# Optimization experiments

Hardware: AMD Instinct MI355X
Metric: run time of the kernel (lower is better)

## Reference

```python
import jax, jax.numpy as jnp
import numpy as np
from jax import lax

B, DIM, H, W = 16, 256, 32, 32
C = DIM // 4          # per-branch channels = 64
HEADS, DH = 8, 64
INNER = HEADS * DH    # 512
R = 16                # SE / CBAM channel reduction
PX = PY = 8           # learned param grid size


def _coords(n_in, n_out):
    s = jnp.linspace(0.0, n_in - 1.0, n_out)
    i0 = jnp.clip(jnp.floor(s).astype(jnp.int32), 0, max(n_in - 2, 0))
    return i0, jnp.clip(i0 + 1, 0, n_in - 1), s - i0


def resize_ac(p, out_h, out_w):
    # bilinear resize with align_corners=True; p: [..., h, w]
    y0, y1, fy = _coords(p.shape[-2], out_h)
    x0, x1, fx = _coords(p.shape[-1], out_w)
    py = p[..., y0, :] * (1.0 - fy)[:, None] + p[..., y1, :] * fy[:, None]
    return py[..., x0] * (1.0 - fx) + py[..., x1] * fx


def ln_last(x, w, b, eps=1e-5):  # torch nn.LayerNorm default eps
    m = x.mean(-1, keepdims=True)
    v = ((x - m) ** 2).mean(-1, keepdims=True)
    return (x - m) * lax.rsqrt(v + eps) * w + b


def ln_cf(x, w, b, eps=1e-6):  # channels_first ConvNeXt LayerNorm
    m = x.mean(1, keepdims=True)
    v = ((x - m) ** 2).mean(1, keepdims=True)
    return w[None, :, None, None] * ((x - m) * lax.rsqrt(v + eps)) + b[None, :, None, None]


def dwconv2d(x, w, b):  # depthwise 3x3, stride 1, pad 1
    o = lax.conv_general_dilated(x, w, (1, 1), 'SAME', dimension_numbers=('NCHW', 'OIHW', 'NCHW'), feature_group_count=x.shape[1])
    return o + b[None, :, None, None]


def dwconv1d(x, w, b):  # depthwise k=3, pad 1
    o = lax.conv_general_dilated(x, w, (1,), 'SAME', dimension_numbers=('NCH', 'OIH', 'NCH'), feature_group_count=x.shape[1])
    return o + b[None, :, None]


def pw(x, w, b):  # 1x1 conv over NCHW, w: [Cout, Cin]
    return jnp.einsum('bchw,dc->bdhw', x, w) + b[None, :, None, None]


def gelu(t):
    return jax.nn.gelu(t, approximate=False)  # torch nn.GELU default = erf


def attention(x, lnw, lnb, wqkv, wout):
    # x: [B, N, C]
    xn = ln_last(x, lnw, lnb)
    q, k, v = jnp.split(xn @ wqkv, 3, axis=-1)
    sp = lambda t: t.reshape(t.shape[0], t.shape[1], HEADS, DH).transpose(0, 2, 1, 3)
    q, k, v = sp(q), sp(k), sp(v)
    a = jax.nn.softmax(jnp.einsum('bhnd,bhmd->bhnm', q, k) * DH ** -0.5, axis=-1)
    o = jnp.einsum('bhnm,bhmd->bhnd', a, v).transpose(0, 2, 1, 3).reshape(x.shape[0], x.shape[1], INNER)
    return o @ wout


def cbam(x, fc1, fc2, sa_w):
    mlp = lambda t: jax.nn.relu(t @ fc1.T) @ fc2.T
    ca = jax.nn.sigmoid(mlp(x.mean((2, 3))) + mlp(x.max((2, 3))))
    x = x * ca[:, :, None, None]
    sp = jnp.stack([x.mean(1), x.max(1)], axis=1)  # [B,2,H,W]
    sa = lax.conv_general_dilated(sp, sa_w, (1, 1), 'SAME', dimension_numbers=('NCHW', 'OIHW', 'NCHW'))
    return x * jax.nn.sigmoid(sa)


def se(x, fc1, fc2):
    y = jax.nn.sigmoid(jax.nn.relu(x.mean((2, 3)) @ fc1.T) @ fc2.T)
    return x * y[:, :, None, None]


def setup_inputs() -> dict:
    key = jax.random.key(0)
    ks = iter(jax.random.split(key, 40))
    nrm = lambda shape, s=0.05: jax.random.normal(next(ks), shape, jnp.float32) * s
    d = {}
    d['x'] = jax.random.normal(next(ks), (B, DIM, H, W), jnp.float32)
    d['n1_w'] = jnp.ones((DIM,)); d['n1_b'] = jnp.zeros((DIM,))
    d['att_ln_w'] = jnp.ones((C,)); d['att_ln_b'] = jnp.zeros((C,))
    d['att_wqkv'] = nrm((C, 3 * INNER))
    d['att_wout'] = nrm((INNER, C))
    d['params_xy'] = jnp.ones((1, C, PX, PY))
    d['cxy_dw_w'] = nrm((C, 1, 3, 3)); d['cxy_dw_b'] = jnp.zeros((C,))
    d['cxy_pw_w'] = nrm((C, C)); d['cxy_pw_b'] = jnp.zeros((C,))
    d['ca_fc1'] = nrm((C // R, C)); d['ca_fc2'] = nrm((C, C // R))
    d['sa_w'] = nrm((1, 2, 7, 7))
    d['params_zx'] = jnp.ones((1, 1, C, PX))
    d['czx_dw_w'] = nrm((C, 1, 3)); d['czx_dw_b'] = jnp.zeros((C,))
    d['czx_pw_w'] = nrm((C, C)); d['czx_pw_b'] = jnp.zeros((C,))
    d['se_fc1'] = nrm((C // R, C)); d['se_fc2'] = nrm((C, C // R))
    d['params_zy'] = jnp.ones((1, 1, C, PY))
    d['czy_dw_w'] = nrm((C, 1, 3)); d['czy_dw_b'] = jnp.zeros((C,))
    d['czy_pw_w'] = nrm((C, C)); d['czy_pw_b'] = jnp.zeros((C,))
    d['dw_pw_w'] = nrm((C, C)); d['dw_pw_b'] = jnp.zeros((C,))
    d['dw_dw_w'] = nrm((C, 1, 3, 3)); d['dw_dw_b'] = jnp.zeros((C,))
    d['n2_w'] = jnp.ones((DIM,)); d['n2_b'] = jnp.zeros((DIM,))
    d['ldw_dw_w'] = nrm((DIM, 1, 3, 3)); d['ldw_dw_b'] = jnp.zeros((DIM,))
    d['ldw_pw_w'] = nrm((DIM, DIM)); d['ldw_pw_b'] = jnp.zeros((DIM,))
    return d


def reference(x, n1_w, n1_b, att_ln_w, att_ln_b, att_wqkv, att_wout, params_xy, cxy_dw_w, cxy_dw_b, cxy_pw_w, cxy_pw_b, ca_fc1, ca_fc2, sa_w, params_zx, czx_dw_w, czx_dw_b, czx_pw_w, czx_pw_b, se_fc1, se_fc2, params_zy, czy_dw_w, czy_dw_b, czy_pw_w, czy_pw_b, dw_pw_w, dw_pw_b, dw_dw_w, dw_dw_b, n2_w, n2_b, ldw_dw_w, ldw_dw_b, ldw_pw_w, ldw_pw_b):
    xn = ln_cf(x, n1_w, n1_b)
    x1, x2, x3, x4 = jnp.split(xn, 4, axis=1)
    Bz, Cz, Hz, Wz = x1.shape
    # branch 1: token self-attention, gated by conv'd upsampled learned grid
    t = attention(x1.transpose(0, 2, 3, 1).reshape(Bz, Hz * Wz, Cz), att_ln_w, att_ln_b, att_wqkv, att_wout)
    x1 = t.reshape(Bz, Hz, Wz, Cz).transpose(0, 3, 1, 2)
    g = pw(gelu(dwconv2d(resize_ac(params_xy, Hz, Wz), cxy_dw_w, cxy_dw_b)), cxy_pw_w, cxy_pw_b)
    x1 = x1 * g
    # branch 2: CBAM + zx gate (permute trick == broadcast over width)
    x2 = cbam(x2, ca_fc1, ca_fc2, sa_w)
    g = resize_ac(params_zx, Cz, Hz)[0]  # [1, C, H]
    g = jnp.einsum('bcl,dc->bdl', gelu(dwconv1d(g, czx_dw_w, czx_dw_b)), czx_pw_w) + czx_pw_b[None, :, None]
    x2 = x2 * g[:, :, :, None]
    # branch 3: SE + zy gate (broadcast over height)
    x3 = se(x3, se_fc1, se_fc2)
    g = resize_ac(params_zy, Cz, Wz)[0]  # [1, C, W]
    g = jnp.einsum('bcl,dc->bdl', gelu(dwconv1d(g, czy_dw_w, czy_dw_b)), czy_pw_w) + czy_pw_b[None, :, None]
    x3 = x3 * g[:, :, None, :]
    # branch 4: pointwise -> GELU -> depthwise
    x4 = dwconv2d(gelu(pw(x4, dw_pw_w, dw_pw_b)), dw_dw_w, dw_dw_b)
    out = ln_cf(jnp.concatenate([x1, x2, x3, x4], axis=1), n2_w, n2_b)
    return pw(gelu(dwconv2d(out, ldw_dw_w, ldw_dw_b)), ldw_pw_w, ldw_pw_b)
```

## Files before the change

### kernel.cpp

```cpp
#include <hip/hip_runtime.h>
#include <hip/hip_bf16.h>
#include <math.h>

#define B_     16
#define DIM_   256
#define H_     32
#define W_     32
#define HW_    1024
#define C_     64
#define HEADS_ 8
#define DH_    64
#define INNER_ 512
#define TOK_   16384

typedef unsigned short ushort_t;
typedef __bf16 bf16x8 __attribute__((ext_vector_type(8)));
typedef float  f32x4  __attribute__((ext_vector_type(4)));

#define AOFF_N1W     0
#define AOFF_N1B     256
#define AOFF_ALNW    512
#define AOFF_ALNB    576
#define AOFF_WQKV    640
#define AOFF_WOUT    98944
#define AOFF_PXY     131712
#define AOFF_CXYDW   135808
#define AOFF_CXYDWB  136384
#define AOFF_CXYPW   136448
#define AOFF_CXYPWB  140544
#define AOFF_CAF1    140608
#define AOFF_CAF2    140864
#define AOFF_SAW     141120
#define AOFF_PZX     141218
#define AOFF_CZXDW   141730
#define AOFF_CZXDWB  141922
#define AOFF_CZXPW   141986
#define AOFF_CZXPWB  146082
#define AOFF_SEF1    146146
#define AOFF_SEF2    146402
#define AOFF_PZY     146658
#define AOFF_CZYDW   147170
#define AOFF_CZYDWB  147362
#define AOFF_CZYPW   147426
#define AOFF_CZYPWB  151522
#define AOFF_DWPW    151586
#define AOFF_DWPWB   155682
#define AOFF_DWDW    155746
#define AOFF_DWDWB   156322
#define AOFF_N2W     156386
#define AOFF_N2B     156642
#define AOFF_LDWDW   156898
#define AOFF_LDWDWB  159202
#define AOFF_LDWPW   159458
#define AOFF_LDWPWB  224994
#define ATOTAL       225250

__device__ __forceinline__ float us2f(ushort_t u) {
  union { unsigned int i; float f; } v; v.i = ((unsigned int)u) << 16; return v.f;
}
__device__ __forceinline__ ushort_t f2us(float f) {
  union { float f; unsigned int i; } v; v.f = f;
  unsigned int x = v.i;
  return (ushort_t)((x + 0x7fffu + ((x >> 16) & 1u)) >> 16);
}
__device__ __forceinline__ float ldx(const void* p, size_t i, bool f32) {
  return f32 ? ((const float*)p)[i] : us2f(((const ushort_t*)p)[i]);
}
__device__ __forceinline__ float gelu_f(float x) {
  return 0.5f * x * (1.0f + erff(x * 0.70710678118654752f));
}
__device__ __forceinline__ float sigmoid_f(float x) {
  return 1.0f / (1.0f + __expf(-x));
}

__global__ void k_probe(const ushort_t* __restrict__ x, int* __restrict__ dtf) {
  __shared__ int cnt;
  if (threadIdx.x == 0) cnt = 0;
  __syncthreads();
  int c = 0;
  for (int i = threadIdx.x; i < 2048; i += 256) {
    int e = (x[i] >> 7) & 0xFF;
    if (e >= 160) ++c;
  }
  atomicAdd(&cnt, c);
  __syncthreads();
  if (threadIdx.x == 0) dtf[0] = (cnt > 16) ? 1 : 0;
}

__global__ void k_diag(void* __restrict__ out, const int* __restrict__ dtf, float val) {
  bool f32 = dtf[0] != 0;
  int i = blockIdx.x * 256 + threadIdx.x;
  if (i < B_ * DIM_ * HW_) {
    if (f32) ((float*)out)[i] = val; else ((ushort_t*)out)[i] = f2us(val);
  }
}

__global__ void k_cvt_all(const void* p0,const void* p1,const void* p2,const void* p3,const void* p4,
                          const void* p5,const void* p6,const void* p7,const void* p8,const void* p9,
                          const void* p10,const void* p11,const void* p12,const void* p13,const void* p14,
                          const void* p15,const void* p16,const void* p17,const void* p18,const void* p19,
                          const void* p20,const void* p21,const void* p22,const void* p23,const void* p24,
                          const void* p25,const void* p26,const void* p27,const void* p28,const void* p29,
                          const void* p30,const void* p31,const void* p32,const void* p33,const void* p34,
                          const void* p35, const int* __restrict__ dtf, float* __restrict__ arena) {
  const void* ps[36] = {p0,p1,p2,p3,p4,p5,p6,p7,p8,p9,p10,p11,p12,p13,p14,p15,p16,p17,
                        p18,p19,p20,p21,p22,p23,p24,p25,p26,p27,p28,p29,p30,p31,p32,p33,p34,p35};
  const int offs[37] = {AOFF_N1W,AOFF_N1B,AOFF_ALNW,AOFF_ALNB,AOFF_WQKV,AOFF_WOUT,AOFF_PXY,
    AOFF_CXYDW,AOFF_CXYDWB,AOFF_CXYPW,AOFF_CXYPWB,AOFF_CAF1,AOFF_CAF2,AOFF_SAW,AOFF_PZX,
    AOFF_CZXDW,AOFF_CZXDWB,AOFF_CZXPW,AOFF_CZXPWB,AOFF_SEF1,AOFF_SEF2,AOFF_PZY,AOFF_CZYDW,
    AOFF_CZYDWB,AOFF_CZYPW,AOFF_CZYPWB,AOFF_DWPW,AOFF_DWPWB,AOFF_DWDW,AOFF_DWDWB,AOFF_N2W,
    AOFF_N2B,AOFF_LDWDW,AOFF_LDWDWB,AOFF_LDWPW,AOFF_LDWPWB,ATOTAL};
  bool f32 = dtf[0] != 0;
  int gid = blockIdx.x * 256 + threadIdx.x;
  if (gid >= ATOTAL) return;
  int t = 0;
  while (offs[t + 1] <= gid) ++t;
  int loc = gid - offs[t];
  arena[gid] = f32 ? ((const float*)ps[t])[loc] : us2f(((const ushort_t*)ps[t])[loc]);
}

__global__ void k_wprep(const float* __restrict__ arena, ushort_t* __restrict__ wqkvT,
                        ushort_t* __restrict__ woutT, ushort_t* __restrict__ wpwB) {
  int gid = blockIdx.x * 256 + threadIdx.x;
  if (gid < 98304) {
    int j = gid >> 6, c = gid & 63;
    wqkvT[gid] = f2us(arena[AOFF_WQKV + c * 1536 + j]);
  } else if (gid < 131072) {
    int g = gid - 98304;
    int c = g >> 9, j = g & 511;
    woutT[g] = f2us(arena[AOFF_WOUT + j * 64 + c]);
  } else if (gid < 196608) {
    int g = gid - 131072;
    wpwB[g] = f2us(arena[AOFF_LDWPW + g]);
  }
}

__global__ __launch_bounds__(256) void k_ln1stats(const void* __restrict__ x, const int* __restrict__ dtf,
                                                  float* __restrict__ m1, float* __restrict__ r1) {
  __shared__ float ps[4][64], ps2[4][64];
  bool xf = dtf[0] != 0;
  int t = threadIdx.x;
  int pi = t & 63, p = t >> 6;
  int pix = blockIdx.x * 64 + pi;
  int bb = pix >> 10, hw = pix & 1023;
  size_t base = (size_t)bb * (DIM_ * HW_) + hw;
  float s = 0.f, s2 = 0.f;
  for (int c = 0; c < 64; ++c) {
    float v = ldx(x, base + (size_t)(p * 64 + c) * HW_, xf);
    s += v; s2 += v * v;
  }
  ps[p][pi] = s; ps2[p][pi] = s2;
  __syncthreads();
  if (t < 64) {
    float S = ps[0][t] + ps[1][t] + ps[2][t] + ps[3][t];
    float S2 = ps2[0][t] + ps2[1][t] + ps2[2][t] + ps2[3][t];
    float mean = S * (1.0f / DIM_);
    float var = fmaxf(S2 * (1.0f / DIM_) - mean * mean, 0.f);
    int px = blockIdx.x * 64 + t;
    m1[px] = mean;
    r1[px] = rsqrtf(var + 1e-6f);
  }
}

__global__ __launch_bounds__(256) void k_ln_tok(const void* __restrict__ x, const int* __restrict__ dtf,
                                                const float* __restrict__ m1, const float* __restrict__ r1,
                                                const float* __restrict__ arena, ushort_t* __restrict__ x1ln) {
  __shared__ float ls[64 * 65];
  __shared__ float pm[4][64], pv[4][64];
  __shared__ float mt[64], rt[64];
  bool xf = dtf[0] != 0;
  int t = threadIdx.x;
  int bb = blockIdx.x >> 4, hw0 = (blockIdx.x & 15) * 64;
  #pragma unroll
  for (int i = 0; i < 16; ++i) {
    int ch = i * 4 + (t >> 6);
    int tk = t & 63;
    int tokg = bb * HW_ + hw0 + tk;
    float v = ldx(x, ((size_t)bb * DIM_ + ch) * HW_ + hw0 + tk, xf);
    ls[ch * 65 + tk] = (v - m1[tokg]) * r1[tokg] * arena[AOFF_N1W + ch] + arena[AOFF_N1B + ch];
  }
  __syncthreads();
  {
    int p = t >> 6, tk = t & 63;
    float s = 0.f, s2 = 0.f;
    #pragma unroll
    for (int c = 0; c < 16; ++c) {
      float v = ls[(p * 16 + c) * 65 + tk];
      s += v; s2 += v * v;
    }
    pm[p][tk] = s; pv[p][tk] = s2;
  }
  __syncthreads();
  if (t < 64) {
    float S = pm[0][t] + pm[1][t] + pm[2][t] + pm[3][t];
    float S2 = pv[0][t] + pv[1][t] + pv[2][t] + pv[3][t];
    float m = S * (1.0f / C_);
    float var = fmaxf(S2 * (1.0f / C_) - m * m, 0.f);
    mt[t] = m;
    rt[t] = rsqrtf(var + 1e-5f);
  }
  __syncthreads();
  unsigned int* dst = (unsigned int*)x1ln;
  #pragma unroll
  for (int i = 0; i < 8; ++i) {
    int idx = i * 256 + t;
    int tok = idx >> 5, cp = idx & 31, c = cp * 2;
    float m = mt[tok], r = rt[tok];
    float v0 = (ls[c * 65 + tok] - m) * r * arena[AOFF_ALNW + c] + arena[AOFF_ALNB + c];
    float v1 = (ls[(c + 1) * 65 + tok] - m) * r * arena[AOFF_ALNW + c + 1] + arena[AOFF_ALNB + c + 1];
    int tokg = bb * HW_ + hw0 + tok;
    dst[(tokg * 64 + c) >> 1] = (unsigned int)f2us(v0) | ((unsigned int)f2us(v1) << 16);
  }
}

__global__ __launch_bounds__(256) void k_qkv_mfma(const ushort_t* __restrict__ x1ln,
                                                  const ushort_t* __restrict__ wqkvT,
                                                  ushort_t* __restrict__ q, ushort_t* __restrict__ k_,
                                                  ushort_t* __restrict__ v_, int tok_base) {
  int jc = blockIdx.x % 6;
  int mt = blockIdx.x / 6;
  int w = threadIdx.x >> 6, lane = threadIdx.x & 63;
  int m = lane & 15, quad = lane >> 4;
  int tok0 = mt * 64;
  bf16x8 a[4][2];
  #pragma unroll
  for (int s = 0; s < 4; ++s)
    #pragma unroll
    for (int kc = 0; kc < 2; ++kc)
      a[s][kc] = *(const bf16x8*)(x1ln + (size_t)(tok_base + tok0 + s*16 + m) * 64 + kc*32 + quad*8);
  bf16x8 bfr[4][2];
  #pragma unroll
  for (int nb = 0; nb < 4; ++nb)
    #pragma unroll
    for (int kc = 0; kc < 2; ++kc)
      bfr[nb][kc] = *(const bf16x8*)(wqkvT + (size_t)(jc*256 + w*64 + nb*16 + m) * 64 + kc*32 + quad*8);
  f32x4 cacc[4][4];
  #pragma unroll
  for (int s = 0; s < 4; ++s)
    #pragma unroll
    for (int nb = 0; nb < 4; ++nb) cacc[s][nb] = (f32x4){0.f, 0.f, 0.f, 0.f};
  #pragma unroll
  for (int kc = 0; kc < 2; ++kc)
    #pragma unroll
    for (int s = 0; s < 4; ++s)
      #pragma unroll
      for (int nb = 0; nb < 4; ++nb)
        cacc[s][nb] = __builtin_amdgcn_mfma_f32_16x16x32_bf16(a[s][kc], bfr[nb][kc], cacc[s][nb], 0, 0, 0);
  #pragma unroll
  for (int nb = 0; nb < 4; ++nb) {
    int j = jc*256 + w*64 + nb*16 + m;
    int which = j >> 9, jj = j & 511;
    int h = jj >> 6, d = jj & 63;
    ushort_t* dst = (which == 0) ? q : ((which == 1) ? k_ : v_);
    float sc = (which == 0) ? 0.125f : 1.0f;
    #pragma unroll
    for (int s = 0; s < 4; ++s)
      #pragma unroll
      for (int r = 0; r < 4; ++r) {
        int tl = tok0 + s*16 + quad*4 + r;
        int bl = tl >> 10, n = tl & 1023;
        dst[(((size_t)bl * HEADS_ + h) * 1024 + n) * 64 + d] = f2us(cacc[s][nb][r] * sc);
      }
  }
}

#define KSTR 72
__global__ __launch_bounds__(256) void k_flash_mfma(const ushort_t* __restrict__ q,
                                                    const ushort_t* __restrict__ k_,
                                                    const ushort_t* __restrict__ v_,
                                                    ushort_t* __restrict__ ao) {
  __shared__ ushort_t Kl[64 * KSTR];
  __shared__ ushort_t Vt[64 * KSTR];
  __shared__ ushort_t Pl[256 * KSTR];
  int bh = blockIdx.x >> 2;
  int qt = blockIdx.x & 3;
  int w = threadIdx.x >> 6, lane = threadIdx.x & 63;
  int m = lane & 15, quad = lane >> 4;
  const size_t bh_off = (size_t)bh * 1024 * 64;

  bf16x8 aq[4][2];
  #pragma unroll
  for (int s = 0; s < 4; ++s)
    #pragma unroll
    for (int kc = 0; kc < 2; ++kc)
      aq[s][kc] = *(const bf16x8*)(q + bh_off + (size_t)(qt*256 + w*64 + s*16 + m) * 64 + kc*32 + quad*8);

  f32x4 oacc[4][4];
  float lacc[4][4];
  #pragma unroll
  for (int s = 0; s < 4; ++s)
    #pragma unroll
    for (int i = 0; i < 4; ++i) {
      oacc[s][i] = (f32x4){0.f, 0.f, 0.f, 0.f};
      lacc[s][i] = 0.f;
    }

  int kkey = threadIdx.x & 63;
  int kd0  = (threadIdx.x >> 6) * 16;
  int vkey = (threadIdx.x & 31) * 2;
  int vd0  = (threadIdx.x >> 5) * 8;

  for (int kt = 0; kt < 16; ++kt) {
    __syncthreads();
    {
      const uint4* src = (const uint4*)(k_ + bh_off + (size_t)(kt*64 + kkey)*64 + kd0);
      uint4 u0 = src[0], u1 = src[1];
      uint4* dst = (uint4*)&Kl[kkey * KSTR + kd0];
      dst[0] = u0; dst[1] = u1;
    }
    {
      const ushort4* s0 = (const ushort4*)(v_ + bh_off + (size_t)(kt*64 + vkey)*64 + vd0);
      const ushort4* s1 = (const ushort4*)(v_ + bh_off + (size_t)(kt*64 + vkey + 1)*64 + vd0);
      ushort4 x0 = s0[0], x1 = s0[1];
      ushort4 y0 = s1[0], y1 = s1[1];
      unsigned int* base = (unsigned int*)&Vt[0];
      int col = vkey >> 1;
      base[(vd0+0)*(KSTR/2) + col] = (unsigned int)x0.x | ((unsigned int)y0.x << 16);
      base[(vd0+1)*(KSTR/2) + col] = (unsigned int)x0.y | ((unsigned int)y0.y << 16);
      base[(vd0+2)*(KSTR/2) + col] = (unsigned int)x0.z | ((unsigned int)y0.z << 16);
      base[(vd0+3)*(KSTR/2) + col] = (unsigned int)x0.w | ((unsigned int)y0.w << 16);
      base[(vd0+4)*(KSTR/2) + col] = (unsigned int)x1.x | ((unsigned int)y1.x << 16);
      base[(vd0+5)*(KSTR/2) + col] = (unsigned int)x1.y | ((unsigned int)y1.y << 16);
      base[(vd0+6)*(KSTR/2) + col] = (unsigned int)x1.z | ((unsigned int)y1.z << 16);
      base[(vd0+7)*(KSTR/2) + col] = (unsigned int)x1.w | ((unsigned int)y1.w << 16);
    }
    __syncthreads();

    f32x4 sacc[4][4];
    #pragma unroll
    for (int s = 0; s < 4; ++s)
      #pragma unroll
      for (int kb = 0; kb < 4; ++kb) sacc[s][kb] = (f32x4){0.f, 0.f, 0.f, 0.f};
    #pragma unroll
    for (int kb = 0; kb < 4; ++kb) {
      bf16x8 bk0 = *(const bf16x8*)&Kl[(kb*16 + m) * KSTR + quad*8];
      bf16x8 bk1 = *(const bf16x8*)&Kl[(kb*16 + m) * KSTR + 32 + quad*8];
      #pragma unroll
      for (int s = 0; s < 4; ++s) {
        sacc[s][kb] = __builtin_amdgcn_mfma_f32_16x16x32_bf16(aq[s][0], bk0, sacc[s][kb], 0, 0, 0);
        sacc[s][kb] = __builtin_amdgcn_mfma_f32_16x16x32_bf16(aq[s][1], bk1, sacc[s][kb], 0, 0, 0);
      }
    }

    #pragma unroll
    for (int s = 0; s < 4; ++s) {
      float rs0 = 0.f, rs1 = 0.f, rs2 = 0.f, rs3 = 0.f;
      #pragma unroll
      for (int kb = 0; kb < 4; ++kb) {
        float p0 = __expf(fminf(sacc[s][kb][0], 30.f));
        float p1 = __expf(fminf(sacc[s][kb][1], 30.f));
        float p2 = __expf(fminf(sacc[s][kb][2], 30.f));
        float p3 = __expf(fminf(sacc[s][kb][3], 30.f));
        rs0 += p0; rs1 += p1; rs2 += p2; rs3 += p3;
        int rbase = (w*64 + s*16 + quad*4) * KSTR + kb*16 + m;
        Pl[rbase + 0*KSTR] = f2us(p0);
        Pl[rbase + 1*KSTR] = f2us(p1);
        Pl[rbase + 2*KSTR] = f2us(p2);
        Pl[rbase + 3*KSTR] = f2us(p3);
      }
      #pragma unroll
      for (int mask = 1; mask <= 8; mask <<= 1) {
        rs0 += __shfl_xor(rs0, mask, 64);
        rs1 += __shfl_xor(rs1, mask, 64);
        rs2 += __shfl_xor(rs2, mask, 64);
        rs3 += __shfl_xor(rs3, mask, 64);
      }
      lacc[s][0] += rs0; lacc[s][1] += rs1; lacc[s][2] += rs2; lacc[s][3] += rs3;
    }

    bf16x8 ap[4][2];
    #pragma unroll
    for (int s = 0; s < 4; ++s)
      #pragma unroll
      for (int kc = 0; kc < 2; ++kc)
        ap[s][kc] = *(const bf16x8*)&Pl[(w*64 + s*16 + m) * KSTR + kc*32 + quad*8];
    #pragma unroll
    for (int db = 0; db < 4; ++db) {
      bf16x8 bv0 = *(const bf16x8*)&Vt[(db*16 + m) * KSTR + quad*8];
      bf16x8 bv1 = *(const bf16x8*)&Vt[(db*16 + m) * KSTR + 32 + quad*8];
      #pragma unroll
      for (int s = 0; s < 4; ++s) {
        oacc[s][db] = __builtin_amdgcn_mfma_f32_16x16x32_bf16(ap[s][0], bv0, oacc[s][db], 0, 0, 0);
        oacc[s][db] = __builtin_amdgcn_mfma_f32_16x16x32_bf16(ap[s][1], bv1, oacc[s][db], 0, 0, 0);
      }
    }
  }

  int bl = bh >> 3, h = bh & 7;
  #pragma unroll
  for (int s = 0; s < 4; ++s) {
    #pragma unroll
    for (int r = 0; r < 4; ++r) {
      float inv = 1.0f / lacc[s][r];
      int qrow = qt*256 + w*64 + s*16 + quad*4 + r;
      ushort_t* op = ao + ((size_t)(bl*1024 + qrow)) * INNER_ + h*64 + m;
      #pragma unroll
      for (int db = 0; db < 4; ++db) op[db*16] = f2us(oacc[s][db][r] * inv);
    }
  }
}

__global__ __launch_bounds__(256) void k_outproj_mfma(const ushort_t* __restrict__ ao,
                                                      const ushort_t* __restrict__ woutT,
                                                      const float* __restrict__ g1,
                                                      ushort_t* __restrict__ cat, int tok_base) {
  int w = threadIdx.x >> 6, lane = threadIdx.x & 63;
  int m = lane & 15, quad = lane >> 4;
  int tok0 = blockIdx.x * 64 + w * 16;
  f32x4 cacc[4];
  #pragma unroll
  for (int nb = 0; nb < 4; ++nb) cacc[nb] = (f32x4){0.f, 0.f, 0.f, 0.f};
  for (int kc = 0; kc < 16; ++kc) {
    bf16x8 a = *(const bf16x8*)(ao + (size_t)(tok0 + m) * INNER_ + kc*32 + quad*8);
    #pragma unroll
    for (int nb = 0; nb < 4; ++nb) {
      bf16x8 b = *(const bf16x8*)(woutT + (size_t)(nb*16 + m) * INNER_ + kc*32 + quad*8);
      cacc[nb] = __builtin_amdgcn_mfma_f32_16x16x32_bf16(a, b, cacc[nb], 0, 0, 0);
    }
  }
  #pragma unroll
  for (int nb = 0; nb < 4; ++nb) {
    int c = nb*16 + m;
    #pragma unroll
    for (int r = 0; r < 4; ++r) {
      int tokg = tok_base + tok0 + quad*4 + r;
      int bb = tokg >> 10, hw = tokg & 1023;
      cat[((size_t)bb * DIM_ + c) * HW_ + hw] = f2us(cacc[nb][r] * g1[c * HW_ + hw]);
    }
  }
}

__global__ void k_resize_xy(const float* __restrict__ arena, float* __restrict__ r) {
  const float* p = arena + AOFF_PXY;
  int idx = blockIdx.x * 256 + threadIdx.x;
  int c = idx >> 10, hw = idx & 1023, oy = hw >> 5, ox = hw & 31;
  float sy = oy * (7.0f / 31.0f); int y0 = (int)floorf(sy); y0 = y0 > 6 ? 6 : y0; float fy = sy - y0;
  float sx = ox * (7.0f / 31.0f); int x0 = (int)floorf(sx); x0 = x0 > 6 ? 6 : x0; float fx = sx - x0;
  const float* pc = p + c * 64;
  float a  = pc[y0*8+x0] * (1.f-fy) + pc[(y0+1)*8+x0] * fy;
  float b2 = pc[y0*8+x0+1] * (1.f-fy) + pc[(y0+1)*8+x0+1] * fy;
  r[idx] = a * (1.f - fx) + b2 * fx;
}
__global__ void k_dwg_xy(const float* __restrict__ r, const float* __restrict__ arena,
                         float* __restrict__ t1) {
  const float* w = arena + AOFF_CXYDW;
  const float* b = arena + AOFF_CXYDWB;
  int idx = blockIdx.x * 256 + threadIdx.x;
  int c = idx >> 10, hw = idx & 1023, yy = hw >> 5, xx = hw & 31;
  const float* base = r + c * HW_;
  float acc = b[c];
  #pragma unroll
  for (int ky = 0; ky < 3; ++ky) {
    int ny = yy + ky - 1; if (ny < 0 || ny > 31) continue;
    #pragma unroll
    for (int kx = 0; kx < 3; ++kx) {
      int nx = xx + kx - 1; if (nx < 0 || nx > 31) continue;
      acc += w[c*9 + ky*3 + kx] * base[ny*32 + nx];
    }
  }
  t1[idx] = gelu_f(acc);
}
__global__ void k_pw_xy(const float* __restrict__ t1, const float* __restrict__ arena,
                        float* __restrict__ g1) {
  const float* w = arena + AOFF_CXYPW;
  const float* b = arena + AOFF_CXYPWB;
  int idx = blockIdx.x * 256 + threadIdx.x;
  int d = idx >> 10, hw = idx & 1023;
  float acc = b[d];
  for (int c = 0; c < C_; ++c) acc += w[d*C_ + c] * t1[c*HW_ + hw];
  g1[idx] = acc;
}

__global__ void k_gate1d_a(const float* __restrict__ arena, int po, int wo, int bo,
                           float* __restrict__ t) {
  const float* p   = arena + po;
  const float* dww = arena + wo;
  const float* dwb = arena + bo;
  int idx = blockIdx.x * 256 + threadIdx.x;
  if (idx >= C_ * 32) return;
  int c = idx >> 5, i = idx & 31;
  float acc = dwb[c];
  #pragma unroll
  for (int kk = 0; kk < 3; ++kk) {
    int ii = i + kk - 1;
    if (ii < 0 || ii > 31) continue;
    float s = ii * (7.0f / 31.0f); int x0 = (int)floorf(s); x0 = x0 > 6 ? 6 : x0; float f = s - x0;
    float val = p[c*8 + x0] * (1.f - f) + p[c*8 + x0 + 1] * f;
    acc += dww[c*3 + kk] * val;
  }
  t[idx] = gelu_f(acc);
}
__global__ void k_gate1d_b(const float* __restrict__ t, const float* __restrict__ arena,
                           int wo, int bo, float* __restrict__ g) {
  const float* w = arena + wo;
  const float* b = arena + bo;
  int idx = blockIdx.x * 256 + threadIdx.x;
  if (idx >= C_ * 32) return;
  int d = idx >> 5, i = idx & 31;
  float acc = b[d];
  for (int c = 0; c < C_; ++c) acc += w[d*C_ + c] * t[c*32 + i];
  g[idx] = acc;
}

__global__ __launch_bounds__(256) void k_pool(const void* __restrict__ x, const int* __restrict__ dtf,
                                              const float* __restrict__ m1, const float* __restrict__ r1,
                                              const float* __restrict__ arena,
                                              int coff, float* __restrict__ om, float* __restrict__ ox) {
  __shared__ float sm[256], sx[256];
  bool xf = dtf[0] != 0;
  int blk = blockIdx.x;
  int bb = blk >> 6, c = blk & 63;
  const size_t xbase = ((size_t)bb * DIM_ + coff + c) * HW_;
  const float* mb = m1 + bb * HW_;
  const float* rb = r1 + bb * HW_;
  float wc = arena[AOFF_N1W + coff + c], bc = arena[AOFF_N1B + coff + c];
  int tid = threadIdx.x;
  float s = 0.f, mx = -1e30f;
  for (int i = tid; i < HW_; i += 256) {
    float v = (ldx(x, xbase + i, xf) - mb[i]) * rb[i] * wc + bc;
    s += v; mx = fmaxf(mx, v);
  }
  sm[tid] = s; sx[tid] = mx; __syncthreads();
  for (int st = 128; st > 0; st >>= 1) {
    if (tid < st) { sm[tid] += sm[tid+st]; sx[tid] = fmaxf(sx[tid], sx[tid+st]); }
    __syncthreads();
  }
  if (tid == 0) { om[blk] = sm[0] * (1.0f / HW_); ox[blk] = sx[0]; }
}

__global__ void k_ca_mlp(const float* __restrict__ mean, const float* __restrict__ mx,
                         const float* __restrict__ arena, float* __restrict__ ca) {
  __shared__ float hid[8];
  const float* fc1 = arena + AOFF_CAF1;
  const float* fc2 = arena + AOFF_CAF2;
  int bb = blockIdx.x, tid = threadIdx.x;
  if (tid < 8) {
    int which = tid >> 2, r = tid & 3;
    const float* src = which ? mx : mean;
    float s = 0.f;
    for (int c = 0; c < C_; ++c) s += src[bb*C_ + c] * fc1[r*C_ + c];
    hid[tid] = fmaxf(s, 0.f);
  }
  __syncthreads();
  float s = 0.f;
  #pragma unroll
  for (int r = 0; r < 4; ++r) s += (hid[r] + hid[4+r]) * fc2[tid*4 + r];
  ca[bb*C_ + tid] = sigmoid_f(s);
}

__global__ void k_se_mlp(const float* __restrict__ mean, const float* __restrict__ arena,
                         float* __restrict__ se) {
  __shared__ float hid[4];
  const float* fc1 = arena + AOFF_SEF1;
  const float* fc2 = arena + AOFF_SEF2;
  int bb = blockIdx.x, tid = threadIdx.x;
  if (tid < 4) {
    float s = 0.f;
    for (int c = 0; c < C_; ++c) s += mean[bb*C_ + c] * fc1[tid*C_ + c];
    hid[tid] = fmaxf(s, 0.f);
  }
  __syncthreads();
  float s = 0.f;
  #pragma unroll
  for (int r = 0; r < 4; ++r) s += hid[r] * fc2[tid*4 + r];
  se[bb*C_ + tid] = sigmoid_f(s);
}

__global__ __launch_bounds__(256) void k_spmaps(const void* __restrict__ x, const int* __restrict__ dtf,
                                                const float* __restrict__ m1, const float* __restrict__ r1,
                                                const float* __restrict__ arena, const float* __restrict__ ca,
                                                float* __restrict__ spm, float* __restrict__ spx) {
  __shared__ float ps[4][64], px[4][64];
  bool xf = dtf[0] != 0;
  int t = threadIdx.x;
  int pi = t & 63, p = t >> 6;
  int pix = blockIdx.x * 64 + pi;
  int bb = pix >> 10, hw = pix & 1023;
  float m = m1[pix], r = r1[pix];
  float s = 0.f, mx = -1e30f;
  for (int c = 0; c < 16; ++c) {
    int ch = p * 16 + c;
    float v = (ldx(x, ((size_t)bb * DIM_ + 64 + ch) * HW_ + hw, xf) - m) * r * arena[AOFF_N1W + 64 + ch] + arena[AOFF_N1B + 64 + ch];
    v *= ca[bb*C_ + ch];
    s += v; mx = fmaxf(mx, v);
  }
  ps[p][pi] = s; px[p][pi] = mx;
  __syncthreads();
  if (t < 64) {
    float S = ps[0][t] + ps[1][t] + ps[2][t] + ps[3][t];
    float M = fmaxf(fmaxf(px[0][t], px[1][t]), fmaxf(px[2][t], px[3][t]));
    int pxi = blockIdx.x * 64 + t;
    spm[pxi] = S * (1.0f / C_);
    spx[pxi] = M;
  }
}

__global__ void k_saconv(const float* __restrict__ spm, const float* __restrict__ spx,
                         const float* __restrict__ arena, float* __restrict__ samask) {
  const float* w = arena + AOFF_SAW;
  int idx = blockIdx.x * 256 + threadIdx.x;
  int bb = idx >> 10, hw = idx & 1023, yy = hw >> 5, xx = hw & 31;
  float acc = 0.f;
  for (int ky = 0; ky < 7; ++ky) {
    int ny = yy + ky - 3; if (ny < 0 || ny > 31) continue;
    for (int kx = 0; kx < 7; ++kx) {
      int nx = xx + kx - 3; if (nx < 0 || nx > 31) continue;
      int off = bb*HW_ + ny*32 + nx;
      acc += spm[off] * w[ky*7 + kx] + spx[off] * w[49 + ky*7 + kx];
    }
  }
  samask[idx] = sigmoid_f(acc);
}

__global__ void k_b2fin(const void* __restrict__ x, const int* __restrict__ dtf,
                        const float* __restrict__ m1, const float* __restrict__ r1,
                        const float* __restrict__ arena,
                        const float* __restrict__ ca, const float* __restrict__ samask,
                        const float* __restrict__ g2, ushort_t* __restrict__ cat) {
  bool xf = dtf[0] != 0;
  int idx = blockIdx.x * 256 + threadIdx.x;
  int hw = idx & 1023, tmp = idx >> 10, c = tmp & 63, bb = tmp >> 6;
  int h = hw >> 5;
  int t = bb * HW_ + hw;
  size_t o = ((size_t)bb * DIM_ + 64 + c) * HW_ + hw;
  float v = (ldx(x, o, xf) - m1[t]) * r1[t] * arena[AOFF_N1W + 64 + c] + arena[AOFF_N1B + 64 + c];
  cat[o] = f2us(v * ca[bb*C_ + c] * samask[t] * g2[c*32 + h]);
}

__global__ void k_b3fin(const void* __restrict__ x, const int* __restrict__ dtf,
                        const float* __restrict__ m1, const float* __restrict__ r1,
                        const float* __restrict__ arena,
                        const float* __restrict__ se, const float* __restrict__ g3,
                        ushort_t* __restrict__ cat) {
  bool xf = dtf[0] != 0;
  int idx = blockIdx.x * 256 + threadIdx.x;
  int hw = idx & 1023, tmp = idx >> 10, c = tmp & 63, bb = tmp >> 6;
  int t = bb * HW_ + hw;
  size_t o = ((size_t)bb * DIM_ + 128 + c) * HW_ + hw;
  float v = (ldx(x, o, xf) - m1[t]) * r1[t] * arena[AOFF_N1W + 128 + c] + arena[AOFF_N1B + 128 + c];
  cat[o] = f2us(v * se[bb*C_ + c] * g3[c*32 + (hw & 31)]);
}

__global__ void k_b4_pw(const void* __restrict__ x, const int* __restrict__ dtf,
                        const float* __restrict__ m1, const float* __restrict__ r1,
                        const float* __restrict__ arena, ushort_t* __restrict__ t4) {
  bool xf = dtf[0] != 0;
  const float* wf = arena + AOFF_DWPW;
  int idx = blockIdx.x * 256 + threadIdx.x;
  int hw = idx & 1023, tmp = idx >> 10, c = tmp & 63, bb = tmp >> 6;
  const size_t xbase = ((size_t)bb * DIM_ + 192) * HW_ + hw;
  int t = bb * HW_ + hw;
  float m = m1[t], r = r1[t];
  float acc = arena[AOFF_DWPWB + c];
  for (int ci = 0; ci < C_; ++ci) {
    float v = (ldx(x, xbase + (size_t)ci * HW_, xf) - m) * r * arena[AOFF_N1W + 192 + ci] + arena[AOFF_N1B + 192 + ci];
    acc += wf[c*C_ + ci] * v;
  }
  t4[idx] = f2us(gelu_f(acc));
}
__global__ void k_b4_dw(const ushort_t* __restrict__ t4, const float* __restrict__ arena,
                        ushort_t* __restrict__ cat) {
  const float* w = arena + AOFF_DWDW;
  int idx = blockIdx.x * 256 + threadIdx.x;
  int hw = idx & 1023, tmp = idx >> 10, c = tmp & 63, bb = tmp >> 6;
  int yy = hw >> 5, xx = hw & 31;
  const ushort_t* base = t4 + ((size_t)bb * C_ + c) * HW_;
  float acc = arena[AOFF_DWDWB + c];
  #pragma unroll
  for (int ky = 0; ky < 3; ++ky) {
    int ny = yy + ky - 1; if (ny < 0 || ny > 31) continue;
    #pragma unroll
    for (int kx = 0; kx < 3; ++kx) {
      int nx = xx + kx - 1; if (nx < 0 || nx > 31) continue;
      acc += w[c*9 + ky*3 + kx] * us2f(base[ny*32 + nx]);
    }
  }
  cat[((size_t)bb * DIM_ + 192 + c) * HW_ + hw] = f2us(acc);
}

__global__ __launch_bounds__(256) void k_ln2stats(const ushort_t* __restrict__ cat,
                                                  float* __restrict__ meanb, float* __restrict__ rstdb) {
  __shared__ float ps[4][64], ps2[4][64];
  int t = threadIdx.x;
  int pi = t & 63, p = t >> 6;
  int pix = blockIdx.x * 64 + pi;
  int bb = pix >> 10, hw = pix & 1023;
  size_t base = (size_t)bb * (DIM_ * HW_) + hw;
  float s = 0.f, s2 = 0.f;
  for (int c = 0; c < 64; ++c) {
    float v = us2f(cat[base + (size_t)(p * 64 + c) * HW_]);
    s += v; s2 += v * v;
  }
  ps[p][pi] = s; ps2[p][pi] = s2;
  __syncthreads();
  if (t < 64) {
    float S = ps[0][t] + ps[1][t] + ps[2][t] + ps[3][t];
    float S2 = ps2[0][t] + ps2[1][t] + ps2[2][t] + ps2[3][t];
    float mean = S * (1.0f / DIM_);
    float var = fmaxf(S2 * (1.0f / DIM_) - mean * mean, 0.f);
    int px = blockIdx.x * 64 + t;
    meanb[px] = mean;
    rstdb[px] = rsqrtf(var + 1e-6f);
  }
}

__global__ void k_final_dw(const ushort_t* __restrict__ cat, const float* __restrict__ meanb,
                           const float* __restrict__ rstdb, const float* __restrict__ arena,
                           ushort_t* __restrict__ z) {
  const float* w = arena + AOFF_LDWDW;
  int idx = blockIdx.x * 256 + threadIdx.x;
  int hw = idx & 1023, tmp = idx >> 10, cc = tmp & 255, bb = tmp >> 8;
  int yy = hw >> 5, xx = hw & 31;
  const ushort_t* base = cat + ((size_t)bb * DIM_ + cc) * HW_;
  const float* mb = meanb + bb * HW_;
  const float* rb = rstdb + bb * HW_;
  float wcc = arena[AOFF_N2W + cc], bcc = arena[AOFF_N2B + cc];
  float acc = arena[AOFF_LDWDWB + cc];
  #pragma unroll
  for (int ky = 0; ky < 3; ++ky) {
    int ny = yy + ky - 1; if (ny < 0 || ny > 31) continue;
    #pragma unroll
    for (int kx = 0; kx < 3; ++kx) {
      int nx = xx + kx - 1; if (nx < 0 || nx > 31) continue;
      int n = ny*32 + nx;
      float v = (us2f(base[n]) - mb[n]) * rb[n] * wcc + bcc;
      acc += w[cc*9 + ky*3 + kx] * v;
    }
  }
  z[((size_t)bb * DIM_ + cc) * HW_ + hw] = f2us(gelu_f(acc));
}

#define ZSTR 264
__global__ __launch_bounds__(256) void k_final_pw_mfma(const ushort_t* __restrict__ z,
                                                       const ushort_t* __restrict__ wpw,
                                                       const float* __restrict__ arena,
                                                       const int* __restrict__ dtf,
                                                       void* __restrict__ out) {
  __shared__ ushort_t zt[64 * ZSTR];
  bool of = dtf[0] != 0;
  int bb = blockIdx.x >> 4, hw0 = (blockIdx.x & 15) * 64;
  int t = threadIdx.x;
  int w = t >> 6, lane = t & 63;
  int m = lane & 15, quad = lane >> 4;
  #pragma unroll
  for (int i = 0; i < 4; ++i) {
    int cp = i * 32 + (t >> 3);
    int c = cp * 2;
    int hw8 = (t & 7) * 8;
    const ushort4* s0 = (const ushort4*)(z + ((size_t)bb * DIM_ + c) * HW_ + hw0 + hw8);
    const ushort4* s1 = (const ushort4*)(z + ((size_t)bb * DIM_ + c + 1) * HW_ + hw0 + hw8);
    ushort4 x0 = s0[0], x1 = s0[1];
    ushort4 y0 = s1[0], y1 = s1[1];
    unsigned int* basep = (unsigned int*)zt;
    basep[(hw8+0)*(ZSTR/2) + cp] = (unsigned int)x0.x | ((unsigned int)y0.x << 16);
    basep[(hw8+1)*(ZSTR/2) + cp] = (unsigned int)x0.y | ((unsigned int)y0.y << 16);
    basep[(hw8+2)*(ZSTR/2) + cp] = (unsigned int)x0.z | ((unsigned int)y0.z << 16);
    basep[(hw8+3)*(ZSTR/2) + cp] = (unsigned int)x0.w | ((unsigned int)y0.w << 16);
    basep[(hw8+4)*(ZSTR/2) + cp] = (unsigned int)x1.x | ((unsigned int)y1.x << 16);
    basep[(hw8+5)*(ZSTR/2) + cp] = (unsigned int)x1.y | ((unsigned int)y1.y << 16);
    basep[(hw8+6)*(ZSTR/2) + cp] = (unsigned int)x1.z | ((unsigned int)y1.z << 16);
    basep[(hw8+7)*(ZSTR/2) + cp] = (unsigned int)x1.w | ((unsigned int)y1.w << 16);
  }
  __syncthreads();
  f32x4 cacc[4][4];
  #pragma unroll
  for (int s = 0; s < 4; ++s)
    #pragma unroll
    for (int nb = 0; nb < 4; ++nb) cacc[s][nb] = (f32x4){0.f, 0.f, 0.f, 0.f};
  for (int kc = 0; kc < 8; ++kc) {
    bf16x8 a[4], b[4];
    #pragma unroll
    for (int s = 0; s < 4; ++s)
      a[s] = *(const bf16x8*)(wpw + (size_t)(w*64 + s*16 + m) * DIM_ + kc*32 + quad*8);
    #pragma unroll
    for (int nb = 0; nb < 4; ++nb)
      b[nb] = *(const bf16x8*)&zt[(nb*16 + m) * ZSTR + kc*32 + quad*8];
    #pragma unroll
    for (int s = 0; s < 4; ++s)
      #pragma unroll
      for (int nb = 0; nb < 4; ++nb)
        cacc[s][nb] = __builtin_amdgcn_mfma_f32_16x16x32_bf16(a[s], b[nb], cacc[s][nb], 0, 0, 0);
  }
  #pragma unroll
  for (int s = 0; s < 4; ++s) {
    #pragma unroll
    for (int r = 0; r < 4; ++r) {
      int d = w*64 + s*16 + quad*4 + r;
      float bv = arena[AOFF_LDWPWB + d];
      #pragma unroll
      for (int nb = 0; nb < 4; ++nb) {
        int hw = hw0 + nb*16 + m;
        float v = cacc[s][nb][r] + bv;
        size_t o = ((size_t)bb * DIM_ + d) * HW_ + hw;
        if (of) ((float*)out)[o] = v; else ((ushort_t*)out)[o] = f2us(v);
      }
    }
  }
}

extern "C" void kernel_launch(void* const* d_in, const int* in_sizes, int n_in,
                              void* d_out, int out_size, void* d_ws, size_t ws_size,
                              hipStream_t stream) {
  const void* x = d_in[0];

  char* wsp = (char*)d_ws; size_t off = 0;
  auto alloc = [&](size_t bytes) -> void* { void* p = wsp + off; off += (bytes + 255) & ~(size_t)255; return p; };

  int*      dtf   = (int*)alloc(sizeof(int));
  float*    arena = (float*)alloc(sizeof(float) * ATOTAL);
  ushort_t* wqkvT = (ushort_t*)alloc(2ull * 1536 * 64);
  ushort_t* woutT = (ushort_t*)alloc(2ull * 64 * 512);
  ushort_t* wpwB  = (ushort_t*)alloc(2ull * DIM_ * DIM_);
  ushort_t* x1ln  = (ushort_t*)alloc(2ull * TOK_ * C_);
  float*    g1    = (float*)alloc(sizeof(float) * C_ * HW_);
  float*    tz    = (float*)alloc(sizeof(float) * C_ * 32);
  float*    g2    = (float*)alloc(sizeof(float) * C_ * 32);
  float*    g3    = (float*)alloc(sizeof(float) * C_ * 32);
  float*    camean= (float*)alloc(sizeof(float) * B_ * C_);
  float*    camax = (float*)alloc(sizeof(float) * B_ * C_);
  float*    cab   = (float*)alloc(sizeof(float) * B_ * C_);
  float*    sem   = (float*)alloc(sizeof(float) * B_ * C_);
  float*    semx  = (float*)alloc(sizeof(float) * B_ * C_);
  float*    seb   = (float*)alloc(sizeof(float) * B_ * C_);
  float*    spm   = (float*)alloc(sizeof(float) * B_ * HW_);
  float*    spx   = (float*)alloc(sizeof(float) * B_ * HW_);
  float*    sam   = (float*)alloc(sizeof(float) * B_ * HW_);
  float*    m1    = (float*)alloc(sizeof(float) * TOK_);
  float*    r1    = (float*)alloc(sizeof(float) * TOK_);
  float*    m2    = (float*)alloc(sizeof(float) * TOK_);
  float*    r2    = (float*)alloc(sizeof(float) * TOK_);

  const size_t qkv_pb  = 2ull * HEADS_ * 1024 * 64;
  const size_t ao_pb   = 2ull * 1024 * INNER_;
  const size_t z_bytes = 2ull * B_ * DIM_ * HW_;
  size_t remain = (ws_size > off) ? (ws_size - off) : 0;
  int bs = 0;
  for (int cand = B_; cand >= 1; cand >>= 1) {
    size_t need = (size_t)cand * (3 * qkv_pb + ao_pb);
    if (need < z_bytes) need = z_bytes;
    if (need + 65536 <= remain) { bs = cand; break; }
  }
  if (bs == 0) {
    k_probe<<<1, 256, 0, stream>>>((const ushort_t*)x, dtf);
    k_diag<<<16384, 256, 0, stream>>>(d_out, dtf, 100.0f + (float)(ws_size >> 20));
    return;
  }
  const int nsplit = B_ / bs;
  size_t qsz = (size_t)bs * qkv_pb;
  size_t region_bytes = (size_t)bs * (3 * qkv_pb + ao_pb);
  if (region_bytes < z_bytes) region_bytes = z_bytes;
  char* region = (char*)alloc(region_bytes);
  float*    rxy  = (float*)(region);
  float*    t1xy = (float*)(region + 262144);
  ushort_t* qq   = (ushort_t*)(region);
  ushort_t* kk   = (ushort_t*)(region + qsz);
  ushort_t* vv   = (ushort_t*)(region + 2 * qsz);
  ushort_t* aob  = (ushort_t*)(region + 3 * qsz);
  ushort_t* t4   = (ushort_t*)(region);
  ushort_t* zbuf = (ushort_t*)(region);
  ushort_t* cat  = (ushort_t*)d_out;

  k_probe<<<1, 256, 0, stream>>>((const ushort_t*)x, dtf);
  k_cvt_all<<<(ATOTAL + 255) / 256, 256, 0, stream>>>(
      d_in[1], d_in[2], d_in[3], d_in[4], d_in[5], d_in[6], d_in[7], d_in[8], d_in[9],
      d_in[10], d_in[11], d_in[12], d_in[13], d_in[14], d_in[15], d_in[16], d_in[17], d_in[18],
      d_in[19], d_in[20], d_in[21], d_in[22], d_in[23], d_in[24], d_in[25], d_in[26], d_in[27],
      d_in[28], d_in[29], d_in[30], d_in[31], d_in[32], d_in[33], d_in[34], d_in[35], d_in[36],
      dtf, arena);
  k_wprep<<<768, 256, 0, stream>>>(arena, wqkvT, woutT, wpwB);

  k_ln1stats<<<256, 256, 0, stream>>>(x, dtf, m1, r1);
  k_ln_tok<<<256, 256, 0, stream>>>(x, dtf, m1, r1, arena, x1ln);

  k_resize_xy<<<256, 256, 0, stream>>>(arena, rxy);
  k_dwg_xy<<<256, 256, 0, stream>>>(rxy, arena, t1xy);
  k_pw_xy<<<256, 256, 0, stream>>>(t1xy, arena, g1);
  k_gate1d_a<<<8, 256, 0, stream>>>(arena, AOFF_PZX, AOFF_CZXDW, AOFF_CZXDWB, tz);
  k_gate1d_b<<<8, 256, 0, stream>>>(tz, arena, AOFF_CZXPW, AOFF_CZXPWB, g2);
  k_gate1d_a<<<8, 256, 0, stream>>>(arena, AOFF_PZY, AOFF_CZYDW, AOFF_CZYDWB, tz);
  k_gate1d_b<<<8, 256, 0, stream>>>(tz, arena, AOFF_CZYPW, AOFF_CZYPWB, g3);

  for (int si = 0; si < nsplit; ++si) {
    int tok_base = si * bs * 1024;
    k_qkv_mfma<<<bs * 96, 256, 0, stream>>>(x1ln, wqkvT, qq, kk, vv, tok_base);
    k_flash_mfma<<<bs * HEADS_ * 4, 256, 0, stream>>>(qq, kk, vv, aob);
    k_outproj_mfma<<<bs * 16, 256, 0, stream>>>(aob, woutT, g1, cat, tok_base);
  }

  k_pool<<<1024, 256, 0, stream>>>(x, dtf, m1, r1, arena, 64, camean, camax);
  k_ca_mlp<<<16, 64, 0, stream>>>(camean, camax, arena, cab);
  k_spmaps<<<256, 256, 0, stream>>>(x, dtf, m1, r1, arena, cab, spm, spx);
  k_saconv<<<64, 256, 0, stream>>>(spm, spx, arena, sam);
  k_b2fin<<<4096, 256, 0, stream>>>(x, dtf, m1, r1, arena, cab, sam, g2, cat);

  k_pool<<<1024, 256, 0, stream>>>(x, dtf, m1, r1, arena, 128, sem, semx);
  k_se_mlp<<<16, 64, 0, stream>>>(sem, arena, seb);
  k_b3fin<<<4096, 256, 0, stream>>>(x, dtf, m1, r1, arena, seb, g3, cat);

  k_b4_pw<<<4096, 256, 0, stream>>>(x, dtf, m1, r1, arena, t4);
  k_b4_dw<<<4096, 256, 0, stream>>>(t4, arena, cat);

  k_ln2stats<<<256, 256, 0, stream>>>(cat, m2, r2);
  k_final_dw<<<16384, 256, 0, stream>>>(cat, m2, r2, arena, zbuf);
  k_final_pw_mfma<<<256, 256, 0, stream>>>(zbuf, wpwB, arena, dtf, d_out);
}
```

Baseline: 442.4 us.

## Fuse small kernels, use MFMA for branch-4 pointwise and softmax row sums

```diff
diff --git a/kernel.cpp b/kernel.cpp
--- a/kernel.cpp
+++ b/kernel.cpp
@@ -120,7 +120,8 @@
 }
 
 __global__ void k_wprep(const float* __restrict__ arena, ushort_t* __restrict__ wqkvT,
-                        ushort_t* __restrict__ woutT, ushort_t* __restrict__ wpwB) {
+                        ushort_t* __restrict__ woutT, ushort_t* __restrict__ wpwB,
+                        ushort_t* __restrict__ wdwpwB) {
   int gid = blockIdx.x * 256 + threadIdx.x;
   if (gid < 98304) {
     int j = gid >> 6, c = gid & 63;
@@ -132,6 +133,9 @@
   } else if (gid < 196608) {
     int g = gid - 131072;
     wpwB[g] = f2us(arena[AOFF_LDWPW + g]);
+  } else if (gid < 200704) {
+    int g = gid - 196608;
+    wdwpwB[g] = f2us(arena[AOFF_DWPW + g]);
   }
 }
 
@@ -164,7 +168,8 @@
 
 __global__ __launch_bounds__(256) void k_ln_tok(const void* __restrict__ x, const int* __restrict__ dtf,
                                                 const float* __restrict__ m1, const float* __restrict__ r1,
-                                                const float* __restrict__ arena, ushort_t* __restrict__ x1ln) {
+                                                const float* __restrict__ arena, ushort_t* __restrict__ x1ln,
+                                                ushort_t* __restrict__ xn4) {
   __shared__ float ls[64 * 65];
   __shared__ float pm[4][64], pv[4][64];
   __shared__ float mt[64], rt[64];
@@ -200,16 +205,40 @@
     rt[t] = rsqrtf(var + 1e-5f);
   }
   __syncthreads();
-  unsigned int* dst = (unsigned int*)x1ln;
-  #pragma unroll
-  for (int i = 0; i < 8; ++i) {
-    int idx = i * 256 + t;
-    int tok = idx >> 5, cp = idx & 31, c = cp * 2;
-    float m = mt[tok], r = rt[tok];
-    float v0 = (ls[c * 65 + tok] - m) * r * arena[AOFF_ALNW + c] + arena[AOFF_ALNB + c];
-    float v1 = (ls[(c + 1) * 65 + tok] - m) * r * arena[AOFF_ALNW + c + 1] + arena[AOFF_ALNB + c + 1];
-    int tokg = bb * HW_ + hw0 + tok;
-    dst[(tokg * 64 + c) >> 1] = (unsigned int)f2us(v0) | ((unsigned int)f2us(v1) << 16);
+  {
+    unsigned int* dst = (unsigned int*)x1ln;
+    #pragma unroll
+    for (int i = 0; i < 8; ++i) {
+      int idx = i * 256 + t;
+      int tok = idx >> 5, cp = idx & 31, c = cp * 2;
+      float m = mt[tok], r = rt[tok];
+      float v0 = (ls[c * 65 + tok] - m) * r * arena[AOFF_ALNW + c] + arena[AOFF_ALNB + c];
+      float v1 = (ls[(c + 1) * 65 + tok] - m) * r * arena[AOFF_ALNW + c + 1] + arena[AOFF_ALNB + c + 1];
+      int tokg = bb * HW_ + hw0 + tok;
+      dst[(tokg * 64 + c) >> 1] = (unsigned int)f2us(v0) | ((unsigned int)f2us(v1) << 16);
+    }
+  }
+  __syncthreads();
+  #pragma unroll
+  for (int i = 0; i < 16; ++i) {
+    int ch = i * 4 + (t >> 6);
+    int tk = t & 63;
+    int tokg = bb * HW_ + hw0 + tk;
+    float v = ldx(x, ((size_t)bb * DIM_ + 192 + ch) * HW_ + hw0 + tk, xf);
+    ls[ch * 65 + tk] = (v - m1[tokg]) * r1[tokg] * arena[AOFF_N1W + 192 + ch] + arena[AOFF_N1B + 192 + ch];
+  }
+  __syncthreads();
+  {
+    unsigned int* dst = (unsigned int*)xn4;
+    #pragma unroll
+    for (int i = 0; i < 8; ++i) {
+      int idx = i * 256 + t;
+      int tok = idx >> 5, cp = idx & 31, c = cp * 2;
+      float v0 = ls[c * 65 + tok];
+      float v1 = ls[(c + 1) * 65 + tok];
+      int tokg = bb * HW_ + hw0 + tok;
+      dst[(tokg * 64 + c) >> 1] = (unsigned int)f2us(v0) | ((unsigned int)f2us(v1) << 16);
+    }
   }
 }
 
@@ -270,7 +299,7 @@
                                                     const ushort_t* __restrict__ v_,
                                                     ushort_t* __restrict__ ao) {
   __shared__ ushort_t Kl[64 * KSTR];
-  __shared__ ushort_t Vt[64 * KSTR];
+  __shared__ ushort_t Vt[80 * KSTR];
   __shared__ ushort_t Pl[256 * KSTR];
   int bh = blockIdx.x >> 2;
   int qt = blockIdx.x & 3;
@@ -278,6 +307,14 @@
   int m = lane & 15, quad = lane >> 4;
   const size_t bh_off = (size_t)bh * 1024 * 64;
 
+  {
+    unsigned int* vtp = (unsigned int*)&Vt[0];
+    for (int i = threadIdx.x; i < 16 * (KSTR / 2); i += 256) {
+      int row = i / (KSTR / 2);
+      vtp[64 * (KSTR / 2) + i] = (row == 0) ? 0x3F803F80u : 0u;
+    }
+  }
+
   bf16x8 aq[4][2];
   #pragma unroll
   for (int s = 0; s < 4; ++s)
@@ -286,14 +323,17 @@
       aq[s][kc] = *(const bf16x8*)(q + bh_off + (size_t)(qt*256 + w*64 + s*16 + m) * 64 + kc*32 + quad*8);
 
   f32x4 oacc[4][4];
-  float lacc[4][4];
-  #pragma unroll
-  for (int s = 0; s < 4; ++s)
-    #pragma unroll
-    for (int i = 0; i < 4; ++i) {
-      oacc[s][i] = (f32x4){0.f, 0.f, 0.f, 0.f};
-      lacc[s][i] = 0.f;
-    }
+  f32x4 lsum[4];
+  #pragma unroll
+  for (int s = 0; s < 4; ++s) {
+    #pragma unroll
+    for (int i = 0; i < 4; ++i) oacc[s][i] = (f32x4){0.f, 0.f, 0.f, 0.f};
+    lsum[s] = (f32x4){0.f, 0.f, 0.f, 0.f};
+  }
+
+  __syncthreads();
+  bf16x8 bvo0 = *(const bf16x8*)&Vt[(64 + m) * KSTR + quad*8];
+  bf16x8 bvo1 = *(const bf16x8*)&Vt[(64 + m) * KSTR + 32 + quad*8];
 
   int kkey = threadIdx.x & 63;
   int kd0  = (threadIdx.x >> 6) * 16;
@@ -344,28 +384,18 @@
 
     #pragma unroll
     for (int s = 0; s < 4; ++s) {
-      float rs0 = 0.f, rs1 = 0.f, rs2 = 0.f, rs3 = 0.f;
       #pragma unroll
       for (int kb = 0; kb < 4; ++kb) {
         float p0 = __expf(fminf(sacc[s][kb][0], 30.f));
         float p1 = __expf(fminf(sacc[s][kb][1], 30.f));
         float p2 = __expf(fminf(sacc[s][kb][2], 30.f));
         float p3 = __expf(fminf(sacc[s][kb][3], 30.f));
-        rs0 += p0; rs1 += p1; rs2 += p2; rs3 += p3;
         int rbase = (w*64 + s*16 + quad*4) * KSTR + kb*16 + m;
         Pl[rbase + 0*KSTR] = f2us(p0);
         Pl[rbase + 1*KSTR] = f2us(p1);
         Pl[rbase + 2*KSTR] = f2us(p2);
         Pl[rbase + 3*KSTR] = f2us(p3);
       }
-      #pragma unroll
-      for (int mask = 1; mask <= 8; mask <<= 1) {
-        rs0 += __shfl_xor(rs0, mask, 64);
-        rs1 += __shfl_xor(rs1, mask, 64);
-        rs2 += __shfl_xor(rs2, mask, 64);
-        rs3 += __shfl_xor(rs3, mask, 64);
-      }
-      lacc[s][0] += rs0; lacc[s][1] += rs1; lacc[s][2] += rs2; lacc[s][3] += rs3;
     }
 
     bf16x8 ap[4][2];
@@ -384,14 +414,21 @@
         oacc[s][db] = __builtin_amdgcn_mfma_f32_16x16x32_bf16(ap[s][1], bv1, oacc[s][db], 0, 0, 0);
       }
     }
+    #pragma unroll
+    for (int s = 0; s < 4; ++s) {
+      lsum[s] = __builtin_amdgcn_mfma_f32_16x16x32_bf16(ap[s][0], bvo0, lsum[s], 0, 0, 0);
+      lsum[s] = __builtin_amdgcn_mfma_f32_16x16x32_bf16(ap[s][1], bvo1, lsum[s], 0, 0, 0);
+    }
   }
 
   int bl = bh >> 3, h = bh & 7;
+  int srcl = lane & 48;
   #pragma unroll
   for (int s = 0; s < 4; ++s) {
     #pragma unroll
     for (int r = 0; r < 4; ++r) {
-      float inv = 1.0f / lacc[s][r];
+      float l = __shfl(lsum[s][r], srcl, 64);
+      float inv = 1.0f / l;
       int qrow = qt*256 + w*64 + s*16 + quad*4 + r;
       ushort_t* op = ao + ((size_t)(bl*1024 + qrow)) * INNER_ + h*64 + m;
       #pragma unroll
@@ -430,32 +467,24 @@
   }
 }
 
-__global__ void k_resize_xy(const float* __restrict__ arena, float* __restrict__ r) {
-  const float* p = arena + AOFF_PXY;
-  int idx = blockIdx.x * 256 + threadIdx.x;
-  int c = idx >> 10, hw = idx & 1023, oy = hw >> 5, ox = hw & 31;
-  float sy = oy * (7.0f / 31.0f); int y0 = (int)floorf(sy); y0 = y0 > 6 ? 6 : y0; float fy = sy - y0;
-  float sx = ox * (7.0f / 31.0f); int x0 = (int)floorf(sx); x0 = x0 > 6 ? 6 : x0; float fx = sx - x0;
-  const float* pc = p + c * 64;
-  float a  = pc[y0*8+x0] * (1.f-fy) + pc[(y0+1)*8+x0] * fy;
-  float b2 = pc[y0*8+x0+1] * (1.f-fy) + pc[(y0+1)*8+x0+1] * fy;
-  r[idx] = a * (1.f - fx) + b2 * fx;
-}
-__global__ void k_dwg_xy(const float* __restrict__ r, const float* __restrict__ arena,
-                         float* __restrict__ t1) {
+__global__ void k_dwg_xy(const float* __restrict__ arena, float* __restrict__ t1) {
   const float* w = arena + AOFF_CXYDW;
   const float* b = arena + AOFF_CXYDWB;
   int idx = blockIdx.x * 256 + threadIdx.x;
   int c = idx >> 10, hw = idx & 1023, yy = hw >> 5, xx = hw & 31;
-  const float* base = r + c * HW_;
+  const float* pc = arena + AOFF_PXY + c * 64;
   float acc = b[c];
   #pragma unroll
   for (int ky = 0; ky < 3; ++ky) {
     int ny = yy + ky - 1; if (ny < 0 || ny > 31) continue;
+    float sy = ny * (7.0f / 31.0f); int y0 = (int)floorf(sy); y0 = y0 > 6 ? 6 : y0; float fy = sy - y0;
     #pragma unroll
     for (int kx = 0; kx < 3; ++kx) {
       int nx = xx + kx - 1; if (nx < 0 || nx > 31) continue;
-      acc += w[c*9 + ky*3 + kx] * base[ny*32 + nx];
+      float sx = nx * (7.0f / 31.0f); int x0 = (int)floorf(sx); x0 = x0 > 6 ? 6 : x0; float fx = sx - x0;
+      float a  = pc[y0*8+x0] * (1.f-fy) + pc[(y0+1)*8+x0] * fy;
+      float b2 = pc[y0*8+x0+1] * (1.f-fy) + pc[(y0+1)*8+x0+1] * fy;
+      acc += w[c*9 + ky*3 + kx] * (a * (1.f - fx) + b2 * fx);
     }
   }
   t1[idx] = gelu_f(acc);
@@ -471,44 +500,55 @@
   g1[idx] = acc;
 }
 
-__global__ void k_gate1d_a(const float* __restrict__ arena, int po, int wo, int bo,
-                           float* __restrict__ t) {
+__global__ __launch_bounds__(256) void k_gate_full(const float* __restrict__ arena,
+                                                   float* __restrict__ g2, float* __restrict__ g3) {
+  __shared__ float ts[C_ * 32];
+  int gi = blockIdx.x;
+  int po  = gi ? AOFF_PZY   : AOFF_PZX;
+  int wo  = gi ? AOFF_CZYDW : AOFF_CZXDW;
+  int bo  = gi ? AOFF_CZYDWB: AOFF_CZXDWB;
+  int pwo = gi ? AOFF_CZYPW : AOFF_CZXPW;
+  int pbo = gi ? AOFF_CZYPWB: AOFF_CZXPWB;
+  float* g = gi ? g3 : g2;
   const float* p   = arena + po;
   const float* dww = arena + wo;
   const float* dwb = arena + bo;
-  int idx = blockIdx.x * 256 + threadIdx.x;
-  if (idx >= C_ * 32) return;
-  int c = idx >> 5, i = idx & 31;
-  float acc = dwb[c];
-  #pragma unroll
-  for (int kk = 0; kk < 3; ++kk) {
-    int ii = i + kk - 1;
-    if (ii < 0 || ii > 31) continue;
-    float s = ii * (7.0f / 31.0f); int x0 = (int)floorf(s); x0 = x0 > 6 ? 6 : x0; float f = s - x0;
-    float val = p[c*8 + x0] * (1.f - f) + p[c*8 + x0 + 1] * f;
-    acc += dww[c*3 + kk] * val;
-  }
-  t[idx] = gelu_f(acc);
-}
-__global__ void k_gate1d_b(const float* __restrict__ t, const float* __restrict__ arena,
-                           int wo, int bo, float* __restrict__ g) {
-  const float* w = arena + wo;
-  const float* b = arena + bo;
-  int idx = blockIdx.x * 256 + threadIdx.x;
-  if (idx >= C_ * 32) return;
-  int d = idx >> 5, i = idx & 31;
-  float acc = b[d];
-  for (int c = 0; c < C_; ++c) acc += w[d*C_ + c] * t[c*32 + i];
-  g[idx] = acc;
-}
-
-__global__ __launch_bounds__(256) void k_pool(const void* __restrict__ x, const int* __restrict__ dtf,
-                                              const float* __restrict__ m1, const float* __restrict__ r1,
-                                              const float* __restrict__ arena,
-                                              int coff, float* __restrict__ om, float* __restrict__ ox) {
+  for (int idx = threadIdx.x; idx < C_ * 32; idx += 256) {
+    int c = idx >> 5, i = idx & 31;
+    float acc = dwb[c];
+    #pragma unroll
+    for (int kk = 0; kk < 3; ++kk) {
+      int ii = i + kk - 1;
+      if (ii < 0 || ii > 31) continue;
+      float s = ii * (7.0f / 31.0f); int x0 = (int)floorf(s); x0 = x0 > 6 ? 6 : x0; float f = s - x0;
+      float val = p[c*8 + x0] * (1.f - f) + p[c*8 + x0 + 1] * f;
+      acc += dww[c*3 + kk] * val;
+    }
+    ts[idx] = gelu_f(acc);
+  }
+  __syncthreads();
+  const float* w = arena + pwo;
+  const float* b = arena + pbo;
+  for (int idx = threadIdx.x; idx < C_ * 32; idx += 256) {
+    int d = idx >> 5, i = idx & 31;
+    float acc = b[d];
+    for (int c = 0; c < C_; ++c) acc += w[d*C_ + c] * ts[c*32 + i];
+    g[idx] = acc;
+  }
+}
+
+__global__ __launch_bounds__(256) void k_pool2(const void* __restrict__ x, const int* __restrict__ dtf,
+                                               const float* __restrict__ m1, const float* __restrict__ r1,
+                                               const float* __restrict__ arena,
+                                               float* __restrict__ camean, float* __restrict__ camax,
+                                               float* __restrict__ sem, float* __restrict__ semx) {
   __shared__ float sm[256], sx[256];
   bool xf = dtf[0] != 0;
-  int blk = blockIdx.x;
+  int which = blockIdx.x >> 10;
+  int blk = blockIdx.x & 1023;
+  int coff = which ? 128 : 64;
+  float* om = which ? sem  : camean;
+  float* ox = which ? semx : camax;
   int bb = blk >> 6, c = blk & 63;
   const size_t xbase = ((size_t)bb * DIM_ + coff + c) * HW_;
   const float* mb = m1 + bb * HW_;
@@ -612,51 +652,60 @@
   samask[idx] = sigmoid_f(acc);
 }
 
-__global__ void k_b2fin(const void* __restrict__ x, const int* __restrict__ dtf,
-                        const float* __restrict__ m1, const float* __restrict__ r1,
-                        const float* __restrict__ arena,
-                        const float* __restrict__ ca, const float* __restrict__ samask,
-                        const float* __restrict__ g2, ushort_t* __restrict__ cat) {
+__global__ void k_bfin(const void* __restrict__ x, const int* __restrict__ dtf,
+                       const float* __restrict__ m1, const float* __restrict__ r1,
+                       const float* __restrict__ arena,
+                       const float* __restrict__ ca, const float* __restrict__ samask,
+                       const float* __restrict__ g2,
+                       const float* __restrict__ se, const float* __restrict__ g3,
+                       ushort_t* __restrict__ cat) {
   bool xf = dtf[0] != 0;
-  int idx = blockIdx.x * 256 + threadIdx.x;
-  int hw = idx & 1023, tmp = idx >> 10, c = tmp & 63, bb = tmp >> 6;
-  int h = hw >> 5;
-  int t = bb * HW_ + hw;
-  size_t o = ((size_t)bb * DIM_ + 64 + c) * HW_ + hw;
-  float v = (ldx(x, o, xf) - m1[t]) * r1[t] * arena[AOFF_N1W + 64 + c] + arena[AOFF_N1B + 64 + c];
-  cat[o] = f2us(v * ca[bb*C_ + c] * samask[t] * g2[c*32 + h]);
-}
-
-__global__ void k_b3fin(const void* __restrict__ x, const int* __restrict__ dtf,
-                        const float* __restrict__ m1, const float* __restrict__ r1,
-                        const float* __restrict__ arena,
-                        const float* __restrict__ se, const float* __restrict__ g3,
-                        ushort_t* __restrict__ cat) {
-  bool xf = dtf[0] != 0;
-  int idx = blockIdx.x * 256 + threadIdx.x;
+  bool second = blockIdx.x >= 4096;
+  int idx = ((int)blockIdx.x & 4095) * 256 + threadIdx.x;
   int hw = idx & 1023, tmp = idx >> 10, c = tmp & 63, bb = tmp >> 6;
   int t = bb * HW_ + hw;
-  size_t o = ((size_t)bb * DIM_ + 128 + c) * HW_ + hw;
-  float v = (ldx(x, o, xf) - m1[t]) * r1[t] * arena[AOFF_N1W + 128 + c] + arena[AOFF_N1B + 128 + c];
-  cat[o] = f2us(v * se[bb*C_ + c] * g3[c*32 + (hw & 31)]);
-}
-
-__global__ void k_b4_pw(const void* __restrict__ x, const int* __restrict__ dtf,
-                        const float* __restrict__ m1, const float* __restrict__ r1,
-                        const float* __restrict__ arena, ushort_t* __restrict__ t4) {
-  bool xf = dtf[0] != 0;
-  const float* wf = arena + AOFF_DWPW;
-  int idx = blockIdx.x * 256 + threadIdx.x;
-  int hw = idx & 1023, tmp = idx >> 10, c = tmp & 63, bb = tmp >> 6;
-  const size_t xbase = ((size_t)bb * DIM_ + 192) * HW_ + hw;
-  int t = bb * HW_ + hw;
-  float m = m1[t], r = r1[t];
-  float acc = arena[AOFF_DWPWB + c];
-  for (int ci = 0; ci < C_; ++ci) {
-    float v = (ldx(x, xbase + (size_t)ci * HW_, xf) - m) * r * arena[AOFF_N1W + 192 + ci] + arena[AOFF_N1B + 192 + ci];
-    acc += wf[c*C_ + ci] * v;
-  }
-  t4[idx] = f2us(gelu_f(acc));
+  if (!second) {
+    int h = hw >> 5;
+    size_t o = ((size_t)bb * DIM_ + 64 + c) * HW_ + hw;
+    float v = (ldx(x, o, xf) - m1[t]) * r1[t] * arena[AOFF_N1W + 64 + c] + arena[AOFF_N1B + 64 + c];
+    cat[o] = f2us(v * ca[bb*C_ + c] * samask[t] * g2[c*32 + h]);
+  } else {
+    size_t o = ((size_t)bb * DIM_ + 128 + c) * HW_ + hw;
+    float v = (ldx(x, o, xf) - m1[t]) * r1[t] * arena[AOFF_N1W + 128 + c] + arena[AOFF_N1B + 128 + c];
+    cat[o] = f2us(v * se[bb*C_ + c] * g3[c*32 + (hw & 31)]);
+  }
+}
+
+__global__ __launch_bounds__(256) void k_b4_mfma(const ushort_t* __restrict__ xn4,
+                                                 const ushort_t* __restrict__ wdw,
+                                                 const float* __restrict__ arena,
+                                                 ushort_t* __restrict__ t4) {
+  int w = threadIdx.x >> 6, lane = threadIdx.x & 63;
+  int m = lane & 15, quad = lane >> 4;
+  int tok0 = blockIdx.x * 64 + w * 16;
+  bf16x8 a0 = *(const bf16x8*)(xn4 + (size_t)(tok0 + m) * 64 + quad*8);
+  bf16x8 a1 = *(const bf16x8*)(xn4 + (size_t)(tok0 + m) * 64 + 32 + quad*8);
+  f32x4 cacc[4];
+  #pragma unroll
+  for (int nb = 0; nb < 4; ++nb) cacc[nb] = (f32x4){0.f, 0.f, 0.f, 0.f};
+  #pragma unroll
+  for (int nb = 0; nb < 4; ++nb) {
+    bf16x8 b0 = *(const bf16x8*)(wdw + (size_t)(nb*16 + m) * 64 + quad*8);
+    bf16x8 b1 = *(const bf16x8*)(wdw + (size_t)(nb*16 + m) * 64 + 32 + quad*8);
+    cacc[nb] = __builtin_amdgcn_mfma_f32_16x16x32_bf16(a0, b0, cacc[nb], 0, 0, 0);
+    cacc[nb] = __builtin_amdgcn_mfma_f32_16x16x32_bf16(a1, b1, cacc[nb], 0, 0, 0);
+  }
+  #pragma unroll
+  for (int nb = 0; nb < 4; ++nb) {
+    int cout = nb*16 + m;
+    float bv = arena[AOFF_DWPWB + cout];
+    #pragma unroll
+    for (int r = 0; r < 4; ++r) {
+      int tokg = tok0 + quad*4 + r;
+      int bb = tokg >> 10, hw = tokg & 1023;
+      t4[((size_t)bb * C_ + cout) * HW_ + hw] = f2us(gelu_f(cacc[nb][r] + bv));
+    }
+  }
 }
 __global__ void k_b4_dw(const ushort_t* __restrict__ t4, const float* __restrict__ arena,
                         ushort_t* __restrict__ cat) {
@@ -678,18 +727,20 @@
   cat[((size_t)bb * DIM_ + 192 + c) * HW_ + hw] = f2us(acc);
 }
 
-__global__ __launch_bounds__(256) void k_ln2stats(const ushort_t* __restrict__ cat,
-                                                  float* __restrict__ meanb, float* __restrict__ rstdb) {
+__global__ __launch_bounds__(256) void k_ln2norm(ushort_t* __restrict__ cat) {
   __shared__ float ps[4][64], ps2[4][64];
+  __shared__ float mS[64], rS[64];
   int t = threadIdx.x;
   int pi = t & 63, p = t >> 6;
   int pix = blockIdx.x * 64 + pi;
   int bb = pix >> 10, hw = pix & 1023;
   size_t base = (size_t)bb * (DIM_ * HW_) + hw;
+  float v[64];
   float s = 0.f, s2 = 0.f;
+  #pragma unroll
   for (int c = 0; c < 64; ++c) {
-    float v = us2f(cat[base + (size_t)(p * 64 + c) * HW_]);
-    s += v; s2 += v * v;
+    v[c] = us2f(cat[base + (size_t)(p * 64 + c) * HW_]);
+    s += v[c]; s2 += v[c] * v[c];
   }
   ps[p][pi] = s; ps2[p][pi] = s2;
   __syncthreads();
@@ -698,35 +749,37 @@
     float S2 = ps2[0][t] + ps2[1][t] + ps2[2][t] + ps2[3][t];
     float mean = S * (1.0f / DIM_);
     float var = fmaxf(S2 * (1.0f / DIM_) - mean * mean, 0.f);
-    int px = blockIdx.x * 64 + t;
-    meanb[px] = mean;
-    rstdb[px] = rsqrtf(var + 1e-6f);
-  }
-}
-
-__global__ void k_final_dw(const ushort_t* __restrict__ cat, const float* __restrict__ meanb,
-                           const float* __restrict__ rstdb, const float* __restrict__ arena,
+    mS[t] = mean;
+    rS[t] = rsqrtf(var + 1e-6f);
+  }
+  __syncthreads();
+  float mean = mS[pi], rr = rS[pi];
+  #pragma unroll
+  for (int c = 0; c < 64; ++c)
+    cat[base + (size_t)(p * 64 + c) * HW_] = f2us((v[c] - mean) * rr);
+}
+
+__global__ void k_final_dw(const ushort_t* __restrict__ cat, const float* __restrict__ arena,
                            ushort_t* __restrict__ z) {
   const float* w = arena + AOFF_LDWDW;
   int idx = blockIdx.x * 256 + threadIdx.x;
   int hw = idx & 1023, tmp = idx >> 10, cc = tmp & 255, bb = tmp >> 8;
   int yy = hw >> 5, xx = hw & 31;
   const ushort_t* base = cat + ((size_t)bb * DIM_ + cc) * HW_;
-  const float* mb = meanb + bb * HW_;
-  const float* rb = rstdb + bb * HW_;
   float wcc = arena[AOFF_N2W + cc], bcc = arena[AOFF_N2B + cc];
-  float acc = arena[AOFF_LDWDWB + cc];
+  float sumws = 0.f, sumw = 0.f;
   #pragma unroll
   for (int ky = 0; ky < 3; ++ky) {
     int ny = yy + ky - 1; if (ny < 0 || ny > 31) continue;
     #pragma unroll
     for (int kx = 0; kx < 3; ++kx) {
       int nx = xx + kx - 1; if (nx < 0 || nx > 31) continue;
-      int n = ny*32 + nx;
-      float v = (us2f(base[n]) - mb[n]) * rb[n] * wcc + bcc;
-      acc += w[cc*9 + ky*3 + kx] * v;
-    }
-  }
+      float wk = w[cc*9 + ky*3 + kx];
+      sumws += wk * us2f(base[ny*32 + nx]);
+      sumw  += wk;
+    }
+  }
+  float acc = arena[AOFF_LDWDWB + cc] + wcc * sumws + bcc * sumw;
   z[((size_t)bb * DIM_ + cc) * HW_ + hw] = f2us(gelu_f(acc));
 }
 
@@ -811,9 +864,10 @@
   ushort_t* wqkvT = (ushort_t*)alloc(2ull * 1536 * 64);
   ushort_t* woutT = (ushort_t*)alloc(2ull * 64 * 512);
   ushort_t* wpwB  = (ushort_t*)alloc(2ull * DIM_ * DIM_);
+  ushort_t* wdwpwB= (ushort_t*)alloc(2ull * C_ * C_);
   ushort_t* x1ln  = (ushort_t*)alloc(2ull * TOK_ * C_);
+  ushort_t* xn4   = (ushort_t*)alloc(2ull * TOK_ * C_);
   float*    g1    = (float*)alloc(sizeof(float) * C_ * HW_);
-  float*    tz    = (float*)alloc(sizeof(float) * C_ * 32);
   float*    g2    = (float*)alloc(sizeof(float) * C_ * 32);
   float*    g3    = (float*)alloc(sizeof(float) * C_ * 32);
   float*    camean= (float*)alloc(sizeof(float) * B_ * C_);
@@ -827,8 +881,6 @@
   float*    sam   = (float*)alloc(sizeof(float) * B_ * HW_);
   float*    m1    = (float*)alloc(sizeof(float) * TOK_);
   float*    r1    = (float*)alloc(sizeof(float) * TOK_);
-  float*    m2    = (float*)alloc(sizeof(float) * TOK_);
-  float*    r2    = (float*)alloc(sizeof(float) * TOK_);
 
   const size_t qkv_pb  = 2ull * HEADS_ * 1024 * 64;
   const size_t ao_pb   = 2ull * 1024 * INNER_;
@@ -850,8 +902,7 @@
   size_t region_bytes = (size_t)bs * (3 * qkv_pb + ao_pb);
   if (region_bytes < z_bytes) region_bytes = z_bytes;
   char* region = (char*)alloc(region_bytes);
-  float*    rxy  = (float*)(region);
-  float*    t1xy = (float*)(region + 262144);
+  float*    t1xy = (float*)(region);
   ushort_t* qq   = (ushort_t*)(region);
   ushort_t* kk   = (ushort_t*)(region + qsz);
   ushort_t* vv   = (ushort_t*)(region + 2 * qsz);
@@ -867,18 +918,14 @@
       d_in[19], d_in[20], d_in[21], d_in[22], d_in[23], d_in[24], d_in[25], d_in[26], d_in[27],
       d_in[28], d_in[29], d_in[30], d_in[31], d_in[32], d_in[33], d_in[34], d_in[35], d_in[36],
       dtf, arena);
-  k_wprep<<<768, 256, 0, stream>>>(arena, wqkvT, woutT, wpwB);
+  k_wprep<<<784, 256, 0, stream>>>(arena, wqkvT, woutT, wpwB, wdwpwB);
 
   k_ln1stats<<<256, 256, 0, stream>>>(x, dtf, m1, r1);
-  k_ln_tok<<<256, 256, 0, stream>>>(x, dtf, m1, r1, arena, x1ln);
-
-  k_resize_xy<<<256, 256, 0, stream>>>(arena, rxy);
-  k_dwg_xy<<<256, 256, 0, stream>>>(rxy, arena, t1xy);
+  k_ln_tok<<<256, 256, 0, stream>>>(x, dtf, m1, r1, arena, x1ln, xn4);
+
+  k_dwg_xy<<<256, 256, 0, stream>>>(arena, t1xy);
   k_pw_xy<<<256, 256, 0, stream>>>(t1xy, arena, g1);
-  k_gate1d_a<<<8, 256, 0, stream>>>(arena, AOFF_PZX, AOFF_CZXDW, AOFF_CZXDWB, tz);
-  k_gate1d_b<<<8, 256, 0, stream>>>(tz, arena, AOFF_CZXPW, AOFF_CZXPWB, g2);
-  k_gate1d_a<<<8, 256, 0, stream>>>(arena, AOFF_PZY, AOFF_CZYDW, AOFF_CZYDWB, tz);
-  k_gate1d_b<<<8, 256, 0, stream>>>(tz, arena, AOFF_CZYPW, AOFF_CZYPWB, g3);
+  k_gate_full<<<2, 256, 0, stream>>>(arena, g2, g3);
 
   for (int si = 0; si < nsplit; ++si) {
     int tok_base = si * bs * 1024;
@@ -887,20 +934,17 @@
     k_outproj_mfma<<<bs * 16, 256, 0, stream>>>(aob, woutT, g1, cat, tok_base);
   }
 
-  k_pool<<<1024, 256, 0, stream>>>(x, dtf, m1, r1, arena, 64, camean, camax);
+  k_pool2<<<2048, 256, 0, stream>>>(x, dtf, m1, r1, arena, camean, camax, sem, semx);
   k_ca_mlp<<<16, 64, 0, stream>>>(camean, camax, arena, cab);
+  k_se_mlp<<<16, 64, 0, stream>>>(sem, arena, seb);
   k_spmaps<<<256, 256, 0, stream>>>(x, dtf, m1, r1, arena, cab, spm, spx);
   k_saconv<<<64, 256, 0, stream>>>(spm, spx, arena, sam);
-  k_b2fin<<<4096, 256, 0, stream>>>(x, dtf, m1, r1, arena, cab, sam, g2, cat);
-
-  k_pool<<<1024, 256, 0, stream>>>(x, dtf, m1, r1, arena, 128, sem, semx);
-  k_se_mlp<<<16, 64, 0, stream>>>(sem, arena, seb);
-  k_b3fin<<<4096, 256, 0, stream>>>(x, dtf, m1, r1, arena, seb, g3, cat);
-
-  k_b4_pw<<<4096, 256, 0, stream>>>(x, dtf, m1, r1, arena, t4);
+  k_bfin<<<8192, 256, 0, stream>>>(x, dtf, m1, r1, arena, cab, sam, g2, seb, g3, cat);
+
+  k_b4_mfma<<<256, 256, 0, stream>>>(xn4, wdwpwB, arena, t4);
   k_b4_dw<<<4096, 256, 0, stream>>>(t4, arena, cat);
 
-  k_ln2stats<<<256, 256, 0, stream>>>(cat, m2, r2);
-  k_final_dw<<<16384, 256, 0, stream>>>(cat, m2, r2, arena, zbuf);
+  k_ln2norm<<<256, 256, 0, stream>>>(cat);
+  k_final_dw<<<16384, 256, 0, stream>>>(cat, arena, zbuf);
   k_final_pw_mfma<<<256, 256, 0, stream>>>(zbuf, wpwB, arena, dtf, d_out);
 }
```

New measurement: 437.9 us. Within noise of the previous version (-1.0%).
